# Kernel tuning notes

Hardware: AMD Instinct MI355X
Metric: run time of the kernel (lower is better)

## Reference

```python
import jax, jax.numpy as jnp
import numpy as np

D_MODEL = 1024
NUM_HEADS = 16
DEPTH = D_MODEL // NUM_HEADS
B, S = 2, 2048


def setup_inputs() -> dict:
    key = jax.random.key(0)
    ks = jax.random.split(key, 13)
    sc = 1.0 / np.sqrt(D_MODEL)
    inp = {
        "q": jax.random.normal(ks[0], (B, S, D_MODEL), jnp.float32),
        "k": jax.random.normal(ks[1], (B, S, D_MODEL), jnp.float32),
        "v": jax.random.normal(ks[2], (B, S, D_MODEL), jnp.float32),
        "mask": jax.random.randint(ks[3], (B, 1, S, S), 0, 2).astype(jnp.float32),
        "wq": jax.random.normal(ks[4], (D_MODEL, D_MODEL), jnp.float32) * sc,
        "bq": jnp.zeros((D_MODEL,), jnp.float32),
        "wk": jax.random.normal(ks[5], (D_MODEL, D_MODEL), jnp.float32) * sc,
        "bk": jnp.zeros((D_MODEL,), jnp.float32),
        "wv": jax.random.normal(ks[6], (D_MODEL, D_MODEL), jnp.float32) * sc,
        "bv": jnp.zeros((D_MODEL,), jnp.float32),
        "wo": jax.random.normal(ks[7], (D_MODEL, D_MODEL), jnp.float32) * sc,
        "bo": jnp.zeros((D_MODEL,), jnp.float32),
    }
    return inp


def _split_heads(x):
    # [B,S,D] -> [B,H,S,depth]
    b, s, _ = x.shape
    return x.reshape(b, s, NUM_HEADS, DEPTH).transpose(0, 2, 1, 3)


def reference(q, k, v, mask, wq, bq, wk, bk, wv, bv, wo, bo):
    qh = _split_heads(q @ wq.T + bq)
    kh = _split_heads(k @ wk.T + bk)
    vh = _split_heads(v @ wv.T + bv)
    logits = jnp.einsum("bhqd,bhkd->bhqk", qh, kh) / jnp.sqrt(
        jnp.asarray(DEPTH, jnp.float32))
    logits = logits + mask * (-1e9)
    attn = jax.nn.softmax(logits, axis=-1)
    out = jnp.einsum("bhqk,bhkd->bhqd", attn, vh)
    out = out.transpose(0, 2, 1, 3).reshape(q.shape[0], -1, D_MODEL)
    return out @ wo.T + bo
```

## Files before the change

kernel.cpp:

```cpp
#include <hip/hip_runtime.h>

#define D_MODEL 1024
#define NHEADS  16
#define DEPTH   64
#define BATCH   2
#define SEQ     2048
#define MROWS   (BATCH * SEQ)
#define QSCALE  0.18033688011112042f

typedef unsigned short u16;
typedef unsigned int   u32;
typedef unsigned long long u64;
typedef __bf16 bf16x8 __attribute__((ext_vector_type(8)));
typedef float  f32x4  __attribute__((ext_vector_type(4)));

#if __has_builtin(__builtin_amdgcn_exp2f)
#define EXP2(x) __builtin_amdgcn_exp2f(x)
#else
#define EXP2(x) exp2f(x)
#endif

__device__ __forceinline__ u16 f2b(float f) {
    return __builtin_bit_cast(u16, static_cast<__bf16>(f));
}
__device__ __forceinline__ bf16x8 ldb8(const u16* p) {
    return __builtin_bit_cast(bf16x8, *(const uint4*)p);
}
__device__ __forceinline__ void gload16(const u16* g, u16* l) {
    __builtin_amdgcn_global_load_lds(
        (const __attribute__((address_space(1))) void*)g,
        (__attribute__((address_space(3))) void*)l, 16, 0, 0);
}

__global__ __launch_bounds__(256) void pack_mask(
    const float* __restrict__ mask, u64* __restrict__ bits)
{
    const int w    = blockIdx.x * 4 + (threadIdx.x >> 6);
    const int lane = threadIdx.x & 63;
    float m = mask[(size_t)w * 64 + lane];
    u64 b = __ballot(m > 0.5f);
    if (lane == 0) bits[w] = b;
}

__global__ __launch_bounds__(256) void cvt_bf16(
    const float* __restrict__ q, const float* __restrict__ k, const float* __restrict__ v,
    const float* __restrict__ wq, const float* __restrict__ wk, const float* __restrict__ wv,
    const float* __restrict__ wo,
    u16* __restrict__ xb, u16* __restrict__ wb)
{
    const size_t e = ((size_t)blockIdx.x * 256 + threadIdx.x) * 8;
    const float* src;
    u16* dst;
    size_t off;
    if (e < 12582912) {
        const int a = (int)(e >> 22);
        off = e & 4194303;
        src = (a == 0) ? q : (a == 1) ? k : v;
        dst = xb + ((size_t)a << 22) + off;
    } else {
        const size_t e2 = e - 12582912;
        const int a = (int)(e2 >> 20);
        off = e2 & 1048575;
        src = (a == 0) ? wq : (a == 1) ? wk : (a == 2) ? wv : wo;
        dst = wb + ((size_t)a << 20) + off;
    }
    const float4 f0 = *(const float4*)(src + off);
    const float4 f1 = *(const float4*)(src + off + 4);
    uint4 o;
    o.x = (u32)f2b(f0.x) | ((u32)f2b(f0.y) << 16);
    o.y = (u32)f2b(f0.z) | ((u32)f2b(f0.w) << 16);
    o.z = (u32)f2b(f1.x) | ((u32)f2b(f1.y) << 16);
    o.w = (u32)f2b(f1.z) | ((u32)f2b(f1.w) << 16);
    *(uint4*)dst = o;
}

__global__ __launch_bounds__(256, 3) void proj3_bf16(
    const u16* __restrict__ xb, const u16* __restrict__ wb,
    const float* __restrict__ bq, const float* __restrict__ bk, const float* __restrict__ bv,
    u16* __restrict__ qws, u16* __restrict__ kws, u16* __restrict__ vtws)
{
    __shared__ __align__(16) u16 la[2][128 * 32];
    __shared__ __align__(16) u16 lb[2][128 * 32];

    const int z = blockIdx.z;
    const u16* X = xb + ((size_t)z << 22);
    const u16* W = wb + ((size_t)z << 20);
    const float* Bi = (z == 0) ? bq : (z == 1) ? bk : bv;
    u16* dst       = (z == 0) ? qws : (z == 1) ? kws : vtws;

    const int tid  = threadIdx.x;
    const int wv_  = tid >> 6;
    const int lane = tid & 63;
    const int quad = lane >> 4;
    const int l15  = lane & 15;
    const int bx = blockIdx.y >> 2;
    const int by = (blockIdx.x << 2) | (blockIdx.y & 3);
    const int wm = (wv_ >> 1) * 64;
    const int wn = (wv_ & 1) * 64;

    f32x4 acc[4][4];
    for (int i = 0; i < 4; ++i)
        for (int j = 0; j < 4; ++j)
            acc[i][j] = (f32x4){0.f, 0.f, 0.f, 0.f};

    const int rowA0 = by * 128;
    const int rowB0 = bx * 128;

    const int strow = tid >> 2;
    const int stcol = (tid & 3) * 8;
    const u16* gA0 = &X[(size_t)(rowA0 + strow) * D_MODEL + stcol];
    const u16* gA1 = gA0 + (size_t)64 * D_MODEL;
    const u16* gB0 = &W[(size_t)(rowB0 + strow) * D_MODEL + stcol];
    const u16* gB1 = gB0 + (size_t)64 * D_MODEL;
    const int l0 = tid * 8, l1 = 2048 + tid * 8;

    gload16(gA0, &la[0][l0]);
    gload16(gA1, &la[0][l1]);
    gload16(gB0, &lb[0][l0]);
    gload16(gB1, &lb[0][l1]);
    __syncthreads();

    for (int t = 0; t < 32; ++t) {
        const int buf = t & 1;
        if (t < 31) {
            const int ko = (t + 1) * 32;
            gload16(gA0 + ko, &la[buf ^ 1][l0]);
            gload16(gA1 + ko, &la[buf ^ 1][l1]);
            gload16(gB0 + ko, &lb[buf ^ 1][l0]);
            gload16(gB1 + ko, &lb[buf ^ 1][l1]);
        }
        bf16x8 af[4], bfr[4];
        #pragma unroll
        for (int tt = 0; tt < 4; ++tt) {
            af[tt]  = ldb8(&la[buf][(wm + tt * 16 + l15) * 32 + quad * 8]);
            bfr[tt] = ldb8(&lb[buf][(wn + tt * 16 + l15) * 32 + quad * 8]);
        }
        #pragma unroll
        for (int mt = 0; mt < 4; ++mt)
            #pragma unroll
            for (int nt = 0; nt < 4; ++nt)
                acc[mt][nt] = __builtin_amdgcn_mfma_f32_16x16x32_bf16(af[mt], bfr[nt], acc[mt][nt], 0, 0, 0);
        __syncthreads();
    }

    #pragma unroll
    for (int nt = 0; nt < 4; ++nt) {
        int n = bx * 128 + wn + nt * 16 + l15;
        float bvv = Bi[n];
        int h = n >> 6, d = n & 63;
        #pragma unroll
        for (int mt = 0; mt < 4; ++mt) {
            #pragma unroll
            for (int r = 0; r < 4; ++r) {
                int m = by * 128 + wm + mt * 16 + quad * 4 + r;
                float c = acc[mt][nt][r] + bvv;
                if (z == 0) c *= QSCALE;
                int b = m >> 11, s = m & (SEQ - 1);
                if (z != 2)
                    dst[(((size_t)(b * NHEADS + h) * SEQ) + s) * DEPTH + d] = f2b(c);
                else
                    dst[(((size_t)(b * NHEADS + h) * DEPTH) + d) * SEQ + s] = f2b(c);
            }
        }
    }
}

__global__ __launch_bounds__(256, 3) void proj3_fused(
    const float* __restrict__ q, const float* __restrict__ k, const float* __restrict__ v,
    const float* __restrict__ wq, const float* __restrict__ wk, const float* __restrict__ wv,
    const float* __restrict__ bq, const float* __restrict__ bk, const float* __restrict__ bv,
    u16* __restrict__ qws, u16* __restrict__ kws, u16* __restrict__ vtws)
{
    __shared__ __align__(16) u16 ldsA[128 * 40];
    __shared__ __align__(16) u16 ldsB[128 * 40];

    const int z = blockIdx.z;
    const float* X  = (z == 0) ? q  : (z == 1) ? k  : v;
    const float* W  = (z == 0) ? wq : (z == 1) ? wk : wv;
    const float* Bi = (z == 0) ? bq : (z == 1) ? bk : bv;
    u16* dst        = (z == 0) ? qws : (z == 1) ? kws : vtws;

    const int tid  = threadIdx.x;
    const int wv_  = tid >> 6;
    const int lane = tid & 63;
    const int quad = lane >> 4;
    const int l15  = lane & 15;
    const int bx = blockIdx.y >> 2;
    const int by = (blockIdx.x << 2) | (blockIdx.y & 3);
    const int wm = (wv_ >> 1) * 64;
    const int wn = (wv_ & 1) * 64;

    f32x4 acc[4][4];
    for (int i = 0; i < 4; ++i)
        for (int j = 0; j < 4; ++j)
            acc[i][j] = (f32x4){0.f, 0.f, 0.f, 0.f};

    const int rowA0 = by * 128;
    const int rowB0 = bx * 128;

    const int sr = tid >> 3;
    const int sc = (tid & 7) * 4;

    float4 pa[4], pb[4];
    #pragma unroll
    for (int i = 0; i < 4; ++i) {
        pa[i] = *(const float4*)&X[(size_t)(rowA0 + sr + i * 32) * D_MODEL + sc];
        pb[i] = *(const float4*)&W[(size_t)(rowB0 + sr + i * 32) * D_MODEL + sc];
    }

    for (int it = 0; it < 32; ++it) {
        #pragma unroll
        for (int i = 0; i < 4; ++i) {
            ushort4 ha, hb;
            ha.x = f2b(pa[i].x); ha.y = f2b(pa[i].y); ha.z = f2b(pa[i].z); ha.w = f2b(pa[i].w);
            hb.x = f2b(pb[i].x); hb.y = f2b(pb[i].y); hb.z = f2b(pb[i].z); hb.w = f2b(pb[i].w);
            *(ushort4*)&ldsA[(sr + i * 32) * 40 + sc] = ha;
            *(ushort4*)&ldsB[(sr + i * 32) * 40 + sc] = hb;
        }
        __syncthreads();

        if (it < 31) {
            const int k0 = (it + 1) * 32;
            #pragma unroll
            for (int i = 0; i < 4; ++i) {
                pa[i] = *(const float4*)&X[(size_t)(rowA0 + sr + i * 32) * D_MODEL + k0 + sc];
                pb[i] = *(const float4*)&W[(size_t)(rowB0 + sr + i * 32) * D_MODEL + k0 + sc];
            }
        }

        bf16x8 af[4], bfr[4];
        #pragma unroll
        for (int t = 0; t < 4; ++t) {
            af[t]  = ldb8(&ldsA[(wm + t * 16 + l15) * 40 + quad * 8]);
            bfr[t] = ldb8(&ldsB[(wn + t * 16 + l15) * 40 + quad * 8]);
        }
        #pragma unroll
        for (int mt = 0; mt < 4; ++mt)
            #pragma unroll
            for (int nt = 0; nt < 4; ++nt)
                acc[mt][nt] = __builtin_amdgcn_mfma_f32_16x16x32_bf16(af[mt], bfr[nt], acc[mt][nt], 0, 0, 0);
        __syncthreads();
    }

    #pragma unroll
    for (int nt = 0; nt < 4; ++nt) {
        int n = bx * 128 + wn + nt * 16 + l15;
        float bvv = Bi[n];
        int h = n >> 6, d = n & 63;
        #pragma unroll
        for (int mt = 0; mt < 4; ++mt) {
            #pragma unroll
            for (int r = 0; r < 4; ++r) {
                int m = by * 128 + wm + mt * 16 + quad * 4 + r;
                float c = acc[mt][nt][r] + bvv;
                if (z == 0) c *= QSCALE;
                int b = m >> 11, s = m & (SEQ - 1);
                if (z != 2)
                    dst[(((size_t)(b * NHEADS + h) * SEQ) + s) * DEPTH + d] = f2b(c);
                else
                    dst[(((size_t)(b * NHEADS + h) * DEPTH) + d) * SEQ + s] = f2b(c);
            }
        }
    }
}

__global__ __launch_bounds__(256, 2) void gemm_out_bf16(
    const u16* __restrict__ X, const u16* __restrict__ W,
    const float* __restrict__ bias, float* __restrict__ out)
{
    __shared__ __align__(16) u16 la[2][128 * 32];
    __shared__ __align__(16) u16 lb[2][64 * 32];

    const int tid  = threadIdx.x;
    const int wv_  = tid >> 6;
    const int lane = tid & 63;
    const int quad = lane >> 4;
    const int l15  = lane & 15;
    const int bx = ((blockIdx.y >> 2) << 1) | (blockIdx.x >> 3);
    const int by = ((blockIdx.x & 7) << 2) | (blockIdx.y & 3);
    const int wm = (wv_ >> 1) * 64;
    const int wn = (wv_ & 1) * 32;

    f32x4 acc[4][2];
    for (int i = 0; i < 4; ++i)
        for (int j = 0; j < 2; ++j)
            acc[i][j] = (f32x4){0.f, 0.f, 0.f, 0.f};

    const int rowA0 = by * 128;
    const int rowB0 = bx * 64;

    const int strow = tid >> 2;
    const int stcol = (tid & 3) * 8;
    const u16* gA0 = &X[(size_t)(rowA0 + strow) * D_MODEL + stcol];
    const u16* gA1 = gA0 + (size_t)64 * D_MODEL;
    const u16* gB0 = &W[(size_t)(rowB0 + strow) * D_MODEL + stcol];
    const int l0 = tid * 8, l1 = 2048 + tid * 8;

    gload16(gA0, &la[0][l0]);
    gload16(gA1, &la[0][l1]);
    gload16(gB0, &lb[0][l0]);
    __syncthreads();

    for (int t = 0; t < 32; ++t) {
        const int buf = t & 1;
        if (t < 31) {
            const int ko = (t + 1) * 32;
            gload16(gA0 + ko, &la[buf ^ 1][l0]);
            gload16(gA1 + ko, &la[buf ^ 1][l1]);
            gload16(gB0 + ko, &lb[buf ^ 1][l0]);
        }
        bf16x8 af[4], bfr[2];
        #pragma unroll
        for (int tt = 0; tt < 4; ++tt)
            af[tt] = ldb8(&la[buf][(wm + tt * 16 + l15) * 32 + quad * 8]);
        #pragma unroll
        for (int tt = 0; tt < 2; ++tt)
            bfr[tt] = ldb8(&lb[buf][(wn + tt * 16 + l15) * 32 + quad * 8]);
        #pragma unroll
        for (int mt = 0; mt < 4; ++mt)
            #pragma unroll
            for (int nt = 0; nt < 2; ++nt)
                acc[mt][nt] = __builtin_amdgcn_mfma_f32_16x16x32_bf16(af[mt], bfr[nt], acc[mt][nt], 0, 0, 0);
        __syncthreads();
    }

    #pragma unroll
    for (int nt = 0; nt < 2; ++nt) {
        int n = bx * 64 + wn + nt * 16 + l15;
        float bvv = bias[n];
        #pragma unroll
        for (int mt = 0; mt < 4; ++mt) {
            #pragma unroll
            for (int r = 0; r < 4; ++r) {
                int m = by * 128 + wm + mt * 16 + quad * 4 + r;
                out[(size_t)m * D_MODEL + n] = acc[mt][nt][r] + bvv;
            }
        }
    }
}

__global__ __launch_bounds__(256) void gemm_out_f32(
    const u16* __restrict__ X, const float* __restrict__ W,
    const float* __restrict__ bias, float* __restrict__ out)
{
    __shared__ __align__(16) u16 ldsA[128 * 40];
    __shared__ __align__(16) u16 ldsB[64 * 40];

    const int tid  = threadIdx.x;
    const int wv_  = tid >> 6;
    const int lane = tid & 63;
    const int quad = lane >> 4;
    const int l15  = lane & 15;
    const int bx = ((blockIdx.y >> 2) << 1) | (blockIdx.x >> 3);
    const int by = ((blockIdx.x & 7) << 2) | (blockIdx.y & 3);
    const int wm = (wv_ >> 1) * 64;
    const int wn = (wv_ & 1) * 32;

    f32x4 acc[4][2];
    for (int i = 0; i < 4; ++i)
        for (int j = 0; j < 2; ++j)
            acc[i][j] = (f32x4){0.f, 0.f, 0.f, 0.f};

    const int rowA0 = by * 128;
    const int rowB0 = bx * 64;

    const int ar = tid >> 2, akc = (tid & 3) * 8;
    const int br = tid >> 3, bc = (tid & 7) * 4;

    uint4  paA[2];
    float4 paB[2];
    #pragma unroll
    for (int i = 0; i < 2; ++i) {
        paA[i] = *(const uint4*)&X[(size_t)(rowA0 + ar + i * 64) * D_MODEL + akc];
        paB[i] = *(const float4*)&W[(size_t)(rowB0 + br + i * 32) * D_MODEL + bc];
    }

    for (int it = 0; it < 32; ++it) {
        #pragma unroll
        for (int i = 0; i < 2; ++i) {
            *(uint4*)&ldsA[(ar + i * 64) * 40 + akc] = paA[i];
            ushort4 hb;
            hb.x = f2b(paB[i].x); hb.y = f2b(paB[i].y); hb.z = f2b(paB[i].z); hb.w = f2b(paB[i].w);
            *(ushort4*)&ldsB[(br + i * 32) * 40 + bc] = hb;
        }
        __syncthreads();

        if (it < 31) {
            const int k0 = (it + 1) * 32;
            #pragma unroll
            for (int i = 0; i < 2; ++i) {
                paA[i] = *(const uint4*)&X[(size_t)(rowA0 + ar + i * 64) * D_MODEL + k0 + akc];
                paB[i] = *(const float4*)&W[(size_t)(rowB0 + br + i * 32) * D_MODEL + k0 + bc];
            }
        }

        bf16x8 af[4], bfr[2];
        #pragma unroll
        for (int t = 0; t < 4; ++t)
            af[t] = ldb8(&ldsA[(wm + t * 16 + l15) * 40 + quad * 8]);
        #pragma unroll
        for (int t = 0; t < 2; ++t)
            bfr[t] = ldb8(&ldsB[(wn + t * 16 + l15) * 40 + quad * 8]);
        #pragma unroll
        for (int mt = 0; mt < 4; ++mt)
            #pragma unroll
            for (int nt = 0; nt < 2; ++nt)
                acc[mt][nt] = __builtin_amdgcn_mfma_f32_16x16x32_bf16(af[mt], bfr[nt], acc[mt][nt], 0, 0, 0);
        __syncthreads();
    }

    #pragma unroll
    for (int nt = 0; nt < 2; ++nt) {
        int n = bx * 64 + wn + nt * 16 + l15;
        float bvv = bias[n];
        #pragma unroll
        for (int mt = 0; mt < 4; ++mt) {
            #pragma unroll
            for (int r = 0; r < 4; ++r) {
                int m = by * 128 + wm + mt * 16 + quad * 4 + r;
                out[(size_t)m * D_MODEL + n] = acc[mt][nt][r] + bvv;
            }
        }
    }
}

__global__ __launch_bounds__(256, 2) void flash_attn(
    const u16* __restrict__ Q, const u16* __restrict__ K,
    const u16* __restrict__ Vt, const u64* __restrict__ maskbits,
    u16* __restrict__ O)
{
    __shared__ __align__(16) u16 ldsK[2][64 * 64];
    __shared__ __align__(16) u16 ldsV[2][64 * 64];
    __shared__ __align__(16) u16 ldsP[4][32 * 64];

    const int tid  = threadIdx.x;
    const int wv_  = tid >> 6;
    const int lane = tid & 63;
    const int quad = lane >> 4;
    const int l15  = lane & 15;
    const int bh = ((blockIdx.x & 7) << 2) | (blockIdx.y & 3);
    const int qt = ((blockIdx.y >> 2) << 2) | (blockIdx.x >> 3);
    const int b  = bh >> 4, h = bh & 15;
    const int q0 = qt * 128 + wv_ * 32;

    const u16* Qb = Q  + (size_t)bh * SEQ * DEPTH;
    const u16* Kb = K  + (size_t)bh * SEQ * DEPTH;
    const u16* Vb = Vt + (size_t)bh * DEPTH * SEQ;
    const u64* MB = maskbits + (size_t)b * SEQ * (SEQ / 64);

    const int srow = tid >> 3;
    const int sc8  = tid & 7;
    const int swz  = ((sc8 ^ (srow & 7)) * 8);
    const int kdst0 = srow * 64 + swz;
    const int kdst1 = (srow + 32) * 64 + swz;

    const int xk0 = ((quad ^ (l15 & 7)) * 8);
    const int xk1 = (((4 + quad) ^ (l15 & 7)) * 8);

    bf16x8 aq0[2], aq1[2];
    #pragma unroll
    for (int f = 0; f < 2; ++f) {
        aq0[f] = ldb8(&Qb[(q0 + f * 16 + l15) * DEPTH + quad * 8]);
        aq1[f] = ldb8(&Qb[(q0 + f * 16 + l15) * DEPTH + 32 + quad * 8]);
    }

    bf16x8 vones;
    #pragma unroll
    for (int i = 0; i < 8; ++i) vones[i] = (__bf16)1.0f;

    f32x4 oa[2][4];
    #pragma unroll
    for (int f = 0; f < 2; ++f)
        for (int i = 0; i < 4; ++i) oa[f][i] = (f32x4){0.f, 0.f, 0.f, 0.f};
    f32x4 lacc[2];
    lacc[0] = (f32x4){0.f, 0.f, 0.f, 0.f};
    lacc[1] = (f32x4){0.f, 0.f, 0.f, 0.f};

    u16* myP = ldsP[wv_];

    int wpa[4][4];
    #pragma unroll
    for (int cc = 0; cc < 4; ++cc)
        #pragma unroll
        for (int r = 0; r < 4; ++r) {
            const int row  = quad * 4 + r;
            const int colg = cc * 2 + (l15 >> 3);
            wpa[cc][r] = row * 64 + ((colg ^ (row & 7)) * 8) + (l15 & 7);
        }
    int rp0_[2], rp1_[2];
    #pragma unroll
    for (int f = 0; f < 2; ++f) {
        rp0_[f] = (f * 16 + l15) * 64 + ((quad ^ (l15 & 7)) * 8);
        rp1_[f] = (f * 16 + l15) * 64 + (((4 + quad) ^ (l15 & 7)) * 8);
    }

    uint4 kreg0 = *(const uint4*)&Kb[(size_t)srow * DEPTH + sc8 * 8];
    uint4 kreg1 = *(const uint4*)&Kb[(size_t)(srow + 32) * DEPTH + sc8 * 8];
    uint4 vreg0 = *(const uint4*)&Vb[(size_t)srow * SEQ + sc8 * 8];
    uint4 vreg1 = *(const uint4*)&Vb[(size_t)(srow + 32) * SEQ + sc8 * 8];

    for (int it = 0; it < 32; ++it) {
        const int buf = it & 1;
        u16* Kl = ldsK[buf];
        u16* Vl = ldsV[buf];

        *(uint4*)&Kl[kdst0] = kreg0;
        *(uint4*)&Kl[kdst1] = kreg1;
        *(uint4*)&Vl[kdst0] = vreg0;
        *(uint4*)&Vl[kdst1] = vreg1;
        __syncthreads();

        if (it < 31) {
            const int kb2 = (it + 1) * 64;
            kreg0 = *(const uint4*)&Kb[(size_t)(kb2 + srow) * DEPTH + sc8 * 8];
            kreg1 = *(const uint4*)&Kb[(size_t)(kb2 + srow + 32) * DEPTH + sc8 * 8];
            vreg0 = *(const uint4*)&Vb[(size_t)srow * SEQ + kb2 + sc8 * 8];
            vreg1 = *(const uint4*)&Vb[(size_t)(srow + 32) * SEQ + kb2 + sc8 * 8];
        }

        u32 tlo[2][4], thi[2][4];
        #pragma unroll
        for (int f = 0; f < 2; ++f)
            #pragma unroll
            for (int r = 0; r < 4; ++r) {
                u64 t = MB[(size_t)(q0 + f * 16 + quad * 4 + r) * (SEQ / 64) + it] >> l15;
                tlo[f][r] = (u32)t;
                thi[f][r] = (u32)(t >> 32);
            }

        #pragma unroll
        for (int cc = 0; cc < 4; ++cc) {
            const int row = cc * 16 + l15;
            bf16x8 bk0 = ldb8(&Kl[row * 64 + xk0]);
            bf16x8 bk1 = ldb8(&Kl[row * 64 + xk1]);
            #pragma unroll
            for (int f = 0; f < 2; ++f) {
                f32x4 z = (f32x4){0.f, 0.f, 0.f, 0.f};
                z = __builtin_amdgcn_mfma_f32_16x16x32_bf16(aq0[f], bk0, z, 0, 0, 0);
                z = __builtin_amdgcn_mfma_f32_16x16x32_bf16(aq1[f], bk1, z, 0, 0, 0);
                #pragma unroll
                for (int r = 0; r < 4; ++r) {
                    u32 w   = (cc < 2) ? tlo[f][r] : thi[f][r];
                    u32 bit = (cc & 1) ? ((w >> 16) & 1u) : (w & 1u);
                    float e = EXP2(z[r]);
                    float p = bit ? 0.f : e;
                    myP[wpa[cc][r] + f * 1024] = f2b(p);
                }
            }
        }

        __builtin_amdgcn_wave_barrier();
        __builtin_amdgcn_s_waitcnt(0xc07f);
        __builtin_amdgcn_wave_barrier();
        bf16x8 pa0[2], pa1[2];
        #pragma unroll
        for (int f = 0; f < 2; ++f) {
            pa0[f] = ldb8(&myP[rp0_[f]]);
            pa1[f] = ldb8(&myP[rp1_[f]]);
        }

        #pragma unroll
        for (int f = 0; f < 2; ++f) {
            lacc[f] = __builtin_amdgcn_mfma_f32_16x16x32_bf16(pa0[f], vones, lacc[f], 0, 0, 0);
            lacc[f] = __builtin_amdgcn_mfma_f32_16x16x32_bf16(pa1[f], vones, lacc[f], 0, 0, 0);
        }

        #pragma unroll
        for (int n = 0; n < 4; ++n) {
            const int row = n * 16 + l15;
            bf16x8 bv0 = ldb8(&Vl[row * 64 + xk0]);
            bf16x8 bv1 = ldb8(&Vl[row * 64 + xk1]);
            #pragma unroll
            for (int f = 0; f < 2; ++f) {
                oa[f][n] = __builtin_amdgcn_mfma_f32_16x16x32_bf16(pa0[f], bv0, oa[f][n], 0, 0, 0);
                oa[f][n] = __builtin_amdgcn_mfma_f32_16x16x32_bf16(pa1[f], bv1, oa[f][n], 0, 0, 0);
            }
        }
    }

    #pragma unroll
    for (int f = 0; f < 2; ++f) {
        float inv[4];
        #pragma unroll
        for (int r = 0; r < 4; ++r)
            inv[r] = 1.0f / lacc[f][r];
        #pragma unroll
        for (int n = 0; n < 4; ++n)
            #pragma unroll
            for (int r = 0; r < 4; ++r) {
                int m = q0 + f * 16 + quad * 4 + r;
                O[((size_t)b * SEQ + m) * D_MODEL + h * DEPTH + n * 16 + l15] =
                    f2b(oa[f][n][r] * inv[r]);
            }
    }
}

extern "C" void kernel_launch(void* const* d_in, const int* in_sizes, int n_in,
                              void* d_out, int out_size, void* d_ws, size_t ws_size,
                              hipStream_t stream) {
    const float* q    = (const float*)d_in[0];
    const float* k    = (const float*)d_in[1];
    const float* v    = (const float*)d_in[2];
    const float* mask = (const float*)d_in[3];
    const float* wq   = (const float*)d_in[4];
    const float* bq   = (const float*)d_in[5];
    const float* wk   = (const float*)d_in[6];
    const float* bk   = (const float*)d_in[7];
    const float* wv   = (const float*)d_in[8];
    const float* bv   = (const float*)d_in[9];
    const float* wo   = (const float*)d_in[10];
    const float* bo   = (const float*)d_in[11];

    u16* base = (u16*)d_ws;
    const size_t seg = (size_t)BATCH * NHEADS * SEQ * DEPTH;
    u16* qws  = base;
    u16* kws  = base + seg;
    u16* vtws = base + 2 * seg;
    u16* ows  = base + 3 * seg;
    u64* mbits = (u64*)(base + 4 * seg);
    u16* xb   = base + 4 * seg + 524288;
    u16* wb   = xb + 3 * seg;
    const size_t need_bytes = (4 * seg + 524288 + 3 * seg + 4u * 1048576) * 2;
    const bool bf16path = (ws_size >= need_bytes);

    dim3 blk(256);
    hipLaunchKernelGGL(pack_mask, dim3(BATCH * SEQ * (SEQ / 64) / 4), blk, 0, stream, mask, mbits);

    dim3 gp(D_MODEL / 128, MROWS / 128, 3);
    if (bf16path) {
        hipLaunchKernelGGL(cvt_bf16, dim3(8192), blk, 0, stream,
                           q, k, v, wq, wk, wv, wo, xb, wb);
        hipLaunchKernelGGL(proj3_bf16, gp, blk, 0, stream,
                           xb, wb, bq, bk, bv, qws, kws, vtws);
    } else {
        hipLaunchKernelGGL(proj3_fused, gp, blk, 0, stream,
                           q, k, v, wq, wk, wv, bq, bk, bv, qws, kws, vtws);
    }

    dim3 ga(32, 16);
    hipLaunchKernelGGL(flash_attn, ga, blk, 0, stream, qws, kws, vtws, mbits, ows);

    dim3 go(D_MODEL / 64, MROWS / 128);
    if (bf16path) {
        hipLaunchKernelGGL(gemm_out_bf16, go, blk, 0, stream, ows, wb + 3 * 1048576, bo, (float*)d_out);
    } else {
        hipLaunchKernelGGL(gemm_out_f32, go, blk, 0, stream, ows, wo, bo, (float*)d_out);
    }
}
```

Measured before the change: 285.5 us.

## Split attention across two KV halves and combine partial outputs

Adds a split-KV flash attention kernel that processes each query tile against half of the key sequence, doubling the grid. It writes fp32 partial outputs and row sums, which a new combine kernel adds, normalizes and converts to bf16. The softmax has no running max; it relies on exp2 of the scaled logits staying in range, and row sums come from an MFMA against a ones vector. The intent is more parallelism and occupancy, at the cost of extra global traffic for the fp32 partials, an extra launch, and reuse of the xb workspace region after the projections.

```diff
diff --git a/kernel.cpp b/kernel.cpp
--- a/kernel.cpp
+++ b/kernel.cpp
@@ -424,6 +424,208 @@
     }
 }
 
+__global__ __launch_bounds__(256, 4) void flash_attn_split(
+    const u16* __restrict__ Q, const u16* __restrict__ K,
+    const u16* __restrict__ Vt, const u64* __restrict__ maskbits,
+    float* __restrict__ Opart, float* __restrict__ lpart)
+{
+    __shared__ __align__(16) u16 ldsK[64 * 64];
+    __shared__ __align__(16) u16 ldsV[64 * 64];
+    __shared__ __align__(16) u16 ldsP[4][32 * 64];
+
+    const int tid  = threadIdx.x;
+    const int wv_  = tid >> 6;
+    const int lane = tid & 63;
+    const int quad = lane >> 4;
+    const int l15  = lane & 15;
+    const int bh  = ((blockIdx.x & 7) << 2) | (blockIdx.y & 3);
+    const int qt5 = ((blockIdx.y >> 2) << 2) | (blockIdx.x >> 3);
+    const int qt  = qt5 >> 1;
+    const int kvh = qt5 & 1;
+    const int b  = bh >> 4;
+    const int q0 = qt * 128 + wv_ * 32;
+    const int c0 = kvh * (SEQ / 2);
+
+    const u16* Qb = Q  + (size_t)bh * SEQ * DEPTH;
+    const u16* Kb = K  + (size_t)bh * SEQ * DEPTH;
+    const u16* Vb = Vt + (size_t)bh * DEPTH * SEQ;
+    const u64* MB = maskbits + (size_t)b * SEQ * (SEQ / 64);
+
+    const int srow = tid >> 3;
+    const int sc8  = tid & 7;
+    const int swz  = ((sc8 ^ (srow & 7)) * 8);
+    const int kdst0 = srow * 64 + swz;
+    const int kdst1 = (srow + 32) * 64 + swz;
+
+    const int xk0 = ((quad ^ (l15 & 7)) * 8);
+    const int xk1 = (((4 + quad) ^ (l15 & 7)) * 8);
+
+    bf16x8 aq0[2], aq1[2];
+    #pragma unroll
+    for (int f = 0; f < 2; ++f) {
+        aq0[f] = ldb8(&Qb[(q0 + f * 16 + l15) * DEPTH + quad * 8]);
+        aq1[f] = ldb8(&Qb[(q0 + f * 16 + l15) * DEPTH + 32 + quad * 8]);
+    }
+
+    bf16x8 vones;
+    #pragma unroll
+    for (int i = 0; i < 8; ++i) vones[i] = (__bf16)1.0f;
+
+    f32x4 oa[2][4];
+    #pragma unroll
+    for (int f = 0; f < 2; ++f)
+        for (int i = 0; i < 4; ++i) oa[f][i] = (f32x4){0.f, 0.f, 0.f, 0.f};
+    f32x4 lacc[2];
+    lacc[0] = (f32x4){0.f, 0.f, 0.f, 0.f};
+    lacc[1] = (f32x4){0.f, 0.f, 0.f, 0.f};
+
+    u16* myP = ldsP[wv_];
+
+    int wpa[4][4];
+    #pragma unroll
+    for (int cc = 0; cc < 4; ++cc)
+        #pragma unroll
+        for (int r = 0; r < 4; ++r) {
+            const int row  = quad * 4 + r;
+            const int colg = cc * 2 + (l15 >> 3);
+            wpa[cc][r] = row * 64 + ((colg ^ (row & 7)) * 8) + (l15 & 7);
+        }
+    int rp0_[2], rp1_[2];
+    #pragma unroll
+    for (int f = 0; f < 2; ++f) {
+        rp0_[f] = (f * 16 + l15) * 64 + ((quad ^ (l15 & 7)) * 8);
+        rp1_[f] = (f * 16 + l15) * 64 + (((4 + quad) ^ (l15 & 7)) * 8);
+    }
+
+    uint4 kreg0 = *(const uint4*)&Kb[(size_t)(c0 + srow) * DEPTH + sc8 * 8];
+    uint4 kreg1 = *(const uint4*)&Kb[(size_t)(c0 + srow + 32) * DEPTH + sc8 * 8];
+    uint4 vreg0 = *(const uint4*)&Vb[(size_t)srow * SEQ + c0 + sc8 * 8];
+    uint4 vreg1 = *(const uint4*)&Vb[(size_t)(srow + 32) * SEQ + c0 + sc8 * 8];
+
+    for (int it = 0; it < 16; ++it) {
+        __syncthreads();
+        *(uint4*)&ldsK[kdst0] = kreg0;
+        *(uint4*)&ldsK[kdst1] = kreg1;
+        *(uint4*)&ldsV[kdst0] = vreg0;
+        *(uint4*)&ldsV[kdst1] = vreg1;
+        __syncthreads();
+
+        if (it < 15) {
+            const int cn = c0 + (it + 1) * 64;
+            kreg0 = *(const uint4*)&Kb[(size_t)(cn + srow) * DEPTH + sc8 * 8];
+            kreg1 = *(const uint4*)&Kb[(size_t)(cn + srow + 32) * DEPTH + sc8 * 8];
+            vreg0 = *(const uint4*)&Vb[(size_t)srow * SEQ + cn + sc8 * 8];
+            vreg1 = *(const uint4*)&Vb[(size_t)(srow + 32) * SEQ + cn + sc8 * 8];
+        }
+
+        const int itg = kvh * 16 + it;
+        u32 tlo[2][4], thi[2][4];
+        #pragma unroll
+        for (int f = 0; f < 2; ++f)
+            #pragma unroll
+            for (int r = 0; r < 4; ++r) {
+                u64 t = MB[(size_t)(q0 + f * 16 + quad * 4 + r) * (SEQ / 64) + itg] >> l15;
+                tlo[f][r] = (u32)t;
+                thi[f][r] = (u32)(t >> 32);
+            }
+
+        #pragma unroll
+        for (int cc = 0; cc < 4; ++cc) {
+            const int row = cc * 16 + l15;
+            bf16x8 bk0 = ldb8(&ldsK[row * 64 + xk0]);
+            bf16x8 bk1 = ldb8(&ldsK[row * 64 + xk1]);
+            #pragma unroll
+            for (int f = 0; f < 2; ++f) {
+                f32x4 z = (f32x4){0.f, 0.f, 0.f, 0.f};
+                z = __builtin_amdgcn_mfma_f32_16x16x32_bf16(aq0[f], bk0, z, 0, 0, 0);
+                z = __builtin_amdgcn_mfma_f32_16x16x32_bf16(aq1[f], bk1, z, 0, 0, 0);
+                #pragma unroll
+                for (int r = 0; r < 4; ++r) {
+                    u32 w   = (cc < 2) ? tlo[f][r] : thi[f][r];
+                    u32 bit = (cc & 1) ? ((w >> 16) & 1u) : (w & 1u);
+                    float e = EXP2(z[r]);
+                    float p = bit ? 0.f : e;
+                    myP[wpa[cc][r] + f * 1024] = f2b(p);
+                }
+            }
+        }
+
+        __builtin_amdgcn_wave_barrier();
+        __builtin_amdgcn_s_waitcnt(0xc07f);
+        __builtin_amdgcn_wave_barrier();
+        bf16x8 pa0[2], pa1[2];
+        #pragma unroll
+        for (int f = 0; f < 2; ++f) {
+            pa0[f] = ldb8(&myP[rp0_[f]]);
+            pa1[f] = ldb8(&myP[rp1_[f]]);
+        }
+
+        #pragma unroll
+        for (int f = 0; f < 2; ++f) {
+            lacc[f] = __builtin_amdgcn_mfma_f32_16x16x32_bf16(pa0[f], vones, lacc[f], 0, 0, 0);
+            lacc[f] = __builtin_amdgcn_mfma_f32_16x16x32_bf16(pa1[f], vones, lacc[f], 0, 0, 0);
+        }
+
+        #pragma unroll
+        for (int n = 0; n < 4; ++n) {
+            const int row = n * 16 + l15;
+            bf16x8 bv0 = ldb8(&ldsV[row * 64 + xk0]);
+            bf16x8 bv1 = ldb8(&ldsV[row * 64 + xk1]);
+            #pragma unroll
+            for (int f = 0; f < 2; ++f) {
+                oa[f][n] = __builtin_amdgcn_mfma_f32_16x16x32_bf16(pa0[f], bv0, oa[f][n], 0, 0, 0);
+                oa[f][n] = __builtin_amdgcn_mfma_f32_16x16x32_bf16(pa1[f], bv1, oa[f][n], 0, 0, 0);
+            }
+        }
+    }
+
+    if (l15 == 0) {
+        #pragma unroll
+        for (int f = 0; f < 2; ++f)
+            #pragma unroll
+            for (int r = 0; r < 4; ++r)
+                lpart[(size_t)kvh * 65536 + (size_t)bh * SEQ + q0 + f * 16 + quad * 4 + r] = lacc[f][r];
+    }
+    #pragma unroll
+    for (int f = 0; f < 2; ++f)
+        #pragma unroll
+        for (int n = 0; n < 4; ++n)
+            #pragma unroll
+            for (int r = 0; r < 4; ++r) {
+                const int m = q0 + f * 16 + quad * 4 + r;
+                Opart[(((size_t)kvh * 32 + bh) * SEQ + m) * DEPTH + n * 16 + l15] = oa[f][n][r];
+            }
+}
+
+__global__ __launch_bounds__(256) void combine_o(
+    const float* __restrict__ Op, const float* __restrict__ lp,
+    u16* __restrict__ ows)
+{
+    const size_t idx = ((size_t)blockIdx.x * 256 + threadIdx.x) * 8;
+    const int row = (int)(idx >> 6);
+    const int d0  = (int)(idx & 63);
+    const float* p0 = Op + (size_t)row * 64 + d0;
+    const float4 a0 = *(const float4*)p0;
+    const float4 a1 = *(const float4*)(p0 + 4);
+    const float4 b0 = *(const float4*)(p0 + 4194304);
+    const float4 b1 = *(const float4*)(p0 + 4194308);
+    const float inv = 1.0f / (lp[row] + lp[65536 + row]);
+    const int bh = row >> 11, s = row & 2047;
+    const int b = bh >> 4, h = bh & 15;
+    u16* o = ows + ((size_t)b * SEQ + s) * D_MODEL + h * DEPTH + d0;
+    ushort4 w0, w1;
+    w0.x = f2b((a0.x + b0.x) * inv);
+    w0.y = f2b((a0.y + b0.y) * inv);
+    w0.z = f2b((a0.z + b0.z) * inv);
+    w0.w = f2b((a0.w + b0.w) * inv);
+    w1.x = f2b((a1.x + b1.x) * inv);
+    w1.y = f2b((a1.y + b1.y) * inv);
+    w1.z = f2b((a1.z + b1.z) * inv);
+    w1.w = f2b((a1.w + b1.w) * inv);
+    *(ushort4*)o = w0;
+    *(ushort4*)(o + 4) = w1;
+}
+
 __global__ __launch_bounds__(256, 2) void flash_attn(
     const u16* __restrict__ Q, const u16* __restrict__ K,
     const u16* __restrict__ Vt, const u64* __restrict__ maskbits,
@@ -618,10 +820,15 @@
     u16* vtws = base + 2 * seg;
     u16* ows  = base + 3 * seg;
     u64* mbits = (u64*)(base + 4 * seg);
-    u16* xb   = base + 4 * seg + 524288;
-    u16* wb   = xb + 3 * seg;
-    const size_t need_bytes = (4 * seg + 524288 + 3 * seg + 4u * 1048576) * 2;
-    const bool bf16path = (ws_size >= need_bytes);
+    u16* wb   = base + 4 * seg + 524288;
+    u16* xb   = wb + 4 * 1048576;
+    float* Opart = (float*)xb;
+    float* lpart = Opart + 8388608;
+    const size_t off_xb_u16 = 4 * seg + 524288 + 4 * 1048576;
+    const size_t need_bf16  = (off_xb_u16 + 3 * seg) * 2;
+    const size_t need_split = off_xb_u16 * 2 + (8388608u + 131072u) * 4;
+    const bool bf16path  = (ws_size >= need_bf16);
+    const bool splitpath = bf16path && (ws_size >= need_split);
 
     dim3 blk(256);
     hipLaunchKernelGGL(pack_mask, dim3(BATCH * SEQ * (SEQ / 64) / 4), blk, 0, stream, mask, mbits);
@@ -637,8 +844,15 @@
                            q, k, v, wq, wk, wv, bq, bk, bv, qws, kws, vtws);
     }
 
-    dim3 ga(32, 16);
-    hipLaunchKernelGGL(flash_attn, ga, blk, 0, stream, qws, kws, vtws, mbits, ows);
+    if (splitpath) {
+        dim3 ga(32, 32);
+        hipLaunchKernelGGL(flash_attn_split, ga, blk, 0, stream,
+                           qws, kws, vtws, mbits, Opart, lpart);
+        hipLaunchKernelGGL(combine_o, dim3(2048), blk, 0, stream, Opart, lpart, ows);
+    } else {
+        dim3 ga(32, 16);
+        hipLaunchKernelGGL(flash_attn, ga, blk, 0, stream, qws, kws, vtws, mbits, ows);
+    }
 
     dim3 go(D_MODEL / 64, MROWS / 128);
     if (bf16path) {
```

New measurement: 295.9 us. 1.04x slower.

## Shrink flash-attention query tile, raise occupancy, and coalesce transposed V stores via LDS

Applied to the files above, without the earlier changes.

Flash attention now gives each wave 16 query rows instead of 32, doubling the grid and raising launch bounds to 4 blocks per CU. The intent is more parallelism and occupancy on the attention stage. The cost is that each K/V tile loaded into LDS is reused by half as many queries. Separately, the bf16 projection stages the V output tile through swizzled LDS so the transposed V layout is written with 16-byte coalesced stores instead of scattered 2-byte writes. The workspace order of the bf16 weight and activation buffers is also swapped.

```diff
diff --git a/kernel.cpp b/kernel.cpp
--- a/kernel.cpp
+++ b/kernel.cpp
@@ -79,8 +79,9 @@
     const float* __restrict__ bq, const float* __restrict__ bk, const float* __restrict__ bv,
     u16* __restrict__ qws, u16* __restrict__ kws, u16* __restrict__ vtws)
 {
-    __shared__ __align__(16) u16 la[2][128 * 32];
-    __shared__ __align__(16) u16 lb[2][128 * 32];
+    __shared__ __align__(16) u16 smem[16384];
+    u16 (*la)[4096] = reinterpret_cast<u16(*)[4096]>(smem);
+    u16 (*lb)[4096] = reinterpret_cast<u16(*)[4096]>(smem + 8192);
 
     const int z = blockIdx.z;
     const u16* X = xb + ((size_t)z << 22);
@@ -143,6 +144,134 @@
         __syncthreads();
     }
 
+    if (z != 2) {
+        #pragma unroll
+        for (int nt = 0; nt < 4; ++nt) {
+            int n = rowB0 + wn + nt * 16 + l15;
+            float bvv = Bi[n];
+            int h = n >> 6, d = n & 63;
+            #pragma unroll
+            for (int mt = 0; mt < 4; ++mt) {
+                #pragma unroll
+                for (int r = 0; r < 4; ++r) {
+                    int m = rowA0 + wm + mt * 16 + quad * 4 + r;
+                    float c = acc[mt][nt][r] + bvv;
+                    if (z == 0) c *= QSCALE;
+                    int b = m >> 11, s = m & (SEQ - 1);
+                    dst[(((size_t)(b * NHEADS + h) * SEQ) + s) * DEPTH + d] = f2b(c);
+                }
+            }
+        }
+    } else {
+        #pragma unroll
+        for (int nt = 0; nt < 4; ++nt) {
+            const int nl = wn + nt * 16 + l15;
+            const float bvv = Bi[rowB0 + nl];
+            #pragma unroll
+            for (int mt = 0; mt < 4; ++mt) {
+                #pragma unroll
+                for (int r2 = 0; r2 < 4; r2 += 2) {
+                    const int ml = wm + mt * 16 + quad * 4 + r2;
+                    u32 pk = (u32)f2b(acc[mt][nt][r2] + bvv)
+                           | ((u32)f2b(acc[mt][nt][r2 + 1] + bvv) << 16);
+                    const int g = ml >> 3;
+                    *(u32*)&smem[nl * 128 + (((g ^ (nl & 15)) << 3) | (ml & 7))] = pk;
+                }
+            }
+        }
+        __syncthreads();
+        const int nl  = tid >> 1;
+        const int cc0 = (tid & 1) * 64;
+        const int n   = rowB0 + nl;
+        const int bb  = rowA0 >> 11;
+        u16* dbase = dst + (((size_t)(bb * NHEADS + (n >> 6)) * DEPTH) + (n & 63)) * SEQ
+                   + (rowA0 & (SEQ - 1)) + cc0;
+        #pragma unroll
+        for (int j = 0; j < 8; ++j) {
+            const int g = (tid & 1) * 8 + j;
+            *(uint4*)&dbase[j * 8] =
+                *(const uint4*)&smem[nl * 128 + ((g ^ (nl & 15)) << 3)];
+        }
+    }
+}
+
+__global__ __launch_bounds__(256, 3) void proj3_fused(
+    const float* __restrict__ q, const float* __restrict__ k, const float* __restrict__ v,
+    const float* __restrict__ wq, const float* __restrict__ wk, const float* __restrict__ wv,
+    const float* __restrict__ bq, const float* __restrict__ bk, const float* __restrict__ bv,
+    u16* __restrict__ qws, u16* __restrict__ kws, u16* __restrict__ vtws)
+{
+    __shared__ __align__(16) u16 ldsA[128 * 40];
+    __shared__ __align__(16) u16 ldsB[128 * 40];
+
+    const int z = blockIdx.z;
+    const float* X  = (z == 0) ? q  : (z == 1) ? k  : v;
+    const float* W  = (z == 0) ? wq : (z == 1) ? wk : wv;
+    const float* Bi = (z == 0) ? bq : (z == 1) ? bk : bv;
+    u16* dst        = (z == 0) ? qws : (z == 1) ? kws : vtws;
+
+    const int tid  = threadIdx.x;
+    const int wv_  = tid >> 6;
+    const int lane = tid & 63;
+    const int quad = lane >> 4;
+    const int l15  = lane & 15;
+    const int bx = blockIdx.y >> 2;
+    const int by = (blockIdx.x << 2) | (blockIdx.y & 3);
+    const int wm = (wv_ >> 1) * 64;
+    const int wn = (wv_ & 1) * 64;
+
+    f32x4 acc[4][4];
+    for (int i = 0; i < 4; ++i)
+        for (int j = 0; j < 4; ++j)
+            acc[i][j] = (f32x4){0.f, 0.f, 0.f, 0.f};
+
+    const int rowA0 = by * 128;
+    const int rowB0 = bx * 128;
+
+    const int sr = tid >> 3;
+    const int sc = (tid & 7) * 4;
+
+    float4 pa[4], pb[4];
+    #pragma unroll
+    for (int i = 0; i < 4; ++i) {
+        pa[i] = *(const float4*)&X[(size_t)(rowA0 + sr + i * 32) * D_MODEL + sc];
+        pb[i] = *(const float4*)&W[(size_t)(rowB0 + sr + i * 32) * D_MODEL + sc];
+    }
+
+    for (int it = 0; it < 32; ++it) {
+        #pragma unroll
+        for (int i = 0; i < 4; ++i) {
+            ushort4 ha, hb;
+            ha.x = f2b(pa[i].x); ha.y = f2b(pa[i].y); ha.z = f2b(pa[i].z); ha.w = f2b(pa[i].w);
+            hb.x = f2b(pb[i].x); hb.y = f2b(pb[i].y); hb.z = f2b(pb[i].z); hb.w = f2b(pb[i].w);
+            *(ushort4*)&ldsA[(sr + i * 32) * 40 + sc] = ha;
+            *(ushort4*)&ldsB[(sr + i * 32) * 40 + sc] = hb;
+        }
+        __syncthreads();
+
+        if (it < 31) {
+            const int k0 = (it + 1) * 32;
+            #pragma unroll
+            for (int i = 0; i < 4; ++i) {
+                pa[i] = *(const float4*)&X[(size_t)(rowA0 + sr + i * 32) * D_MODEL + k0 + sc];
+                pb[i] = *(const float4*)&W[(size_t)(rowB0 + sr + i * 32) * D_MODEL + k0 + sc];
+            }
+        }
+
+        bf16x8 af[4], bfr[4];
+        #pragma unroll
+        for (int t = 0; t < 4; ++t) {
+            af[t]  = ldb8(&ldsA[(wm + t * 16 + l15) * 40 + quad * 8]);
+            bfr[t] = ldb8(&ldsB[(wn + t * 16 + l15) * 40 + quad * 8]);
+        }
+        #pragma unroll
+        for (int mt = 0; mt < 4; ++mt)
+            #pragma unroll
+            for (int nt = 0; nt < 4; ++nt)
+                acc[mt][nt] = __builtin_amdgcn_mfma_f32_16x16x32_bf16(af[mt], bfr[nt], acc[mt][nt], 0, 0, 0);
+        __syncthreads();
+    }
+
     #pragma unroll
     for (int nt = 0; nt < 4; ++nt) {
         int n = bx * 128 + wn + nt * 16 + l15;
@@ -165,105 +294,6 @@
     }
 }
 
-__global__ __launch_bounds__(256, 3) void proj3_fused(
-    const float* __restrict__ q, const float* __restrict__ k, const float* __restrict__ v,
-    const float* __restrict__ wq, const float* __restrict__ wk, const float* __restrict__ wv,
-    const float* __restrict__ bq, const float* __restrict__ bk, const float* __restrict__ bv,
-    u16* __restrict__ qws, u16* __restrict__ kws, u16* __restrict__ vtws)
-{
-    __shared__ __align__(16) u16 ldsA[128 * 40];
-    __shared__ __align__(16) u16 ldsB[128 * 40];
-
-    const int z = blockIdx.z;
-    const float* X  = (z == 0) ? q  : (z == 1) ? k  : v;
-    const float* W  = (z == 0) ? wq : (z == 1) ? wk : wv;
-    const float* Bi = (z == 0) ? bq : (z == 1) ? bk : bv;
-    u16* dst        = (z == 0) ? qws : (z == 1) ? kws : vtws;
-
-    const int tid  = threadIdx.x;
-    const int wv_  = tid >> 6;
-    const int lane = tid & 63;
-    const int quad = lane >> 4;
-    const int l15  = lane & 15;
-    const int bx = blockIdx.y >> 2;
-    const int by = (blockIdx.x << 2) | (blockIdx.y & 3);
-    const int wm = (wv_ >> 1) * 64;
-    const int wn = (wv_ & 1) * 64;
-
-    f32x4 acc[4][4];
-    for (int i = 0; i < 4; ++i)
-        for (int j = 0; j < 4; ++j)
-            acc[i][j] = (f32x4){0.f, 0.f, 0.f, 0.f};
-
-    const int rowA0 = by * 128;
-    const int rowB0 = bx * 128;
-
-    const int sr = tid >> 3;
-    const int sc = (tid & 7) * 4;
-
-    float4 pa[4], pb[4];
-    #pragma unroll
-    for (int i = 0; i < 4; ++i) {
-        pa[i] = *(const float4*)&X[(size_t)(rowA0 + sr + i * 32) * D_MODEL + sc];
-        pb[i] = *(const float4*)&W[(size_t)(rowB0 + sr + i * 32) * D_MODEL + sc];
-    }
-
-    for (int it = 0; it < 32; ++it) {
-        #pragma unroll
-        for (int i = 0; i < 4; ++i) {
-            ushort4 ha, hb;
-            ha.x = f2b(pa[i].x); ha.y = f2b(pa[i].y); ha.z = f2b(pa[i].z); ha.w = f2b(pa[i].w);
-            hb.x = f2b(pb[i].x); hb.y = f2b(pb[i].y); hb.z = f2b(pb[i].z); hb.w = f2b(pb[i].w);
-            *(ushort4*)&ldsA[(sr + i * 32) * 40 + sc] = ha;
-            *(ushort4*)&ldsB[(sr + i * 32) * 40 + sc] = hb;
-        }
-        __syncthreads();
-
-        if (it < 31) {
-            const int k0 = (it + 1) * 32;
-            #pragma unroll
-            for (int i = 0; i < 4; ++i) {
-                pa[i] = *(const float4*)&X[(size_t)(rowA0 + sr + i * 32) * D_MODEL + k0 + sc];
-                pb[i] = *(const float4*)&W[(size_t)(rowB0 + sr + i * 32) * D_MODEL + k0 + sc];
-            }
-        }
-
-        bf16x8 af[4], bfr[4];
-        #pragma unroll
-        for (int t = 0; t < 4; ++t) {
-            af[t]  = ldb8(&ldsA[(wm + t * 16 + l15) * 40 + quad * 8]);
-            bfr[t] = ldb8(&ldsB[(wn + t * 16 + l15) * 40 + quad * 8]);
-        }
-        #pragma unroll
-        for (int mt = 0; mt < 4; ++mt)
-            #pragma unroll
-            for (int nt = 0; nt < 4; ++nt)
-                acc[mt][nt] = __builtin_amdgcn_mfma_f32_16x16x32_bf16(af[mt], bfr[nt], acc[mt][nt], 0, 0, 0);
-        __syncthreads();
-    }
-
-    #pragma unroll
-    for (int nt = 0; nt < 4; ++nt) {
-        int n = bx * 128 + wn + nt * 16 + l15;
-        float bvv = Bi[n];
-        int h = n >> 6, d = n & 63;
-        #pragma unroll
-        for (int mt = 0; mt < 4; ++mt) {
-            #pragma unroll
-            for (int r = 0; r < 4; ++r) {
-                int m = by * 128 + wm + mt * 16 + quad * 4 + r;
-                float c = acc[mt][nt][r] + bvv;
-                if (z == 0) c *= QSCALE;
-                int b = m >> 11, s = m & (SEQ - 1);
-                if (z != 2)
-                    dst[(((size_t)(b * NHEADS + h) * SEQ) + s) * DEPTH + d] = f2b(c);
-                else
-                    dst[(((size_t)(b * NHEADS + h) * DEPTH) + d) * SEQ + s] = f2b(c);
-            }
-        }
-    }
-}
-
 __global__ __launch_bounds__(256, 2) void gemm_out_bf16(
     const u16* __restrict__ X, const u16* __restrict__ W,
     const float* __restrict__ bias, float* __restrict__ out)
@@ -424,14 +454,14 @@
     }
 }
 
-__global__ __launch_bounds__(256, 2) void flash_attn(
+__global__ __launch_bounds__(256, 4) void flash_attn(
     const u16* __restrict__ Q, const u16* __restrict__ K,
     const u16* __restrict__ Vt, const u64* __restrict__ maskbits,
     u16* __restrict__ O)
 {
     __shared__ __align__(16) u16 ldsK[2][64 * 64];
     __shared__ __align__(16) u16 ldsV[2][64 * 64];
-    __shared__ __align__(16) u16 ldsP[4][32 * 64];
+    __shared__ __align__(16) u16 ldsP[4][16 * 64];
 
     const int tid  = threadIdx.x;
     const int wv_  = tid >> 6;
@@ -441,7 +471,7 @@
     const int bh = ((blockIdx.x & 7) << 2) | (blockIdx.y & 3);
     const int qt = ((blockIdx.y >> 2) << 2) | (blockIdx.x >> 3);
     const int b  = bh >> 4, h = bh & 15;
-    const int q0 = qt * 128 + wv_ * 32;
+    const int q0 = qt * 64 + wv_ * 16;
 
     const u16* Qb = Q  + (size_t)bh * SEQ * DEPTH;
     const u16* Kb = K  + (size_t)bh * SEQ * DEPTH;
@@ -457,42 +487,30 @@
     const int xk0 = ((quad ^ (l15 & 7)) * 8);
     const int xk1 = (((4 + quad) ^ (l15 & 7)) * 8);
 
-    bf16x8 aq0[2], aq1[2];
-    #pragma unroll
-    for (int f = 0; f < 2; ++f) {
-        aq0[f] = ldb8(&Qb[(q0 + f * 16 + l15) * DEPTH + quad * 8]);
-        aq1[f] = ldb8(&Qb[(q0 + f * 16 + l15) * DEPTH + 32 + quad * 8]);
-    }
+    bf16x8 aq0 = ldb8(&Qb[(q0 + l15) * DEPTH + quad * 8]);
+    bf16x8 aq1 = ldb8(&Qb[(q0 + l15) * DEPTH + 32 + quad * 8]);
 
     bf16x8 vones;
     #pragma unroll
     for (int i = 0; i < 8; ++i) vones[i] = (__bf16)1.0f;
 
-    f32x4 oa[2][4];
-    #pragma unroll
-    for (int f = 0; f < 2; ++f)
-        for (int i = 0; i < 4; ++i) oa[f][i] = (f32x4){0.f, 0.f, 0.f, 0.f};
-    f32x4 lacc[2];
-    lacc[0] = (f32x4){0.f, 0.f, 0.f, 0.f};
-    lacc[1] = (f32x4){0.f, 0.f, 0.f, 0.f};
+    f32x4 oa[4];
+    for (int i = 0; i < 4; ++i) oa[i] = (f32x4){0.f, 0.f, 0.f, 0.f};
+    f32x4 lacc = (f32x4){0.f, 0.f, 0.f, 0.f};
 
     u16* myP = ldsP[wv_];
 
-    int wpa[4][4];
+    int wp[4][4];
     #pragma unroll
     for (int cc = 0; cc < 4; ++cc)
         #pragma unroll
         for (int r = 0; r < 4; ++r) {
             const int row  = quad * 4 + r;
             const int colg = cc * 2 + (l15 >> 3);
-            wpa[cc][r] = row * 64 + ((colg ^ (row & 7)) * 8) + (l15 & 7);
-        }
-    int rp0_[2], rp1_[2];
-    #pragma unroll
-    for (int f = 0; f < 2; ++f) {
-        rp0_[f] = (f * 16 + l15) * 64 + ((quad ^ (l15 & 7)) * 8);
-        rp1_[f] = (f * 16 + l15) * 64 + (((4 + quad) ^ (l15 & 7)) * 8);
-    }
+            wp[cc][r] = row * 64 + ((colg ^ (row & 7)) * 8) + (l15 & 7);
+        }
+    const int rp0 = l15 * 64 + ((quad ^ (l15 & 7)) * 8);
+    const int rp1 = l15 * 64 + (((4 + quad) ^ (l15 & 7)) * 8);
 
     uint4 kreg0 = *(const uint4*)&Kb[(size_t)srow * DEPTH + sc8 * 8];
     uint4 kreg1 = *(const uint4*)&Kb[(size_t)(srow + 32) * DEPTH + sc8 * 8];
@@ -518,81 +536,64 @@
             vreg1 = *(const uint4*)&Vb[(size_t)(srow + 32) * SEQ + kb2 + sc8 * 8];
         }
 
-        u32 tlo[2][4], thi[2][4];
-        #pragma unroll
-        for (int f = 0; f < 2; ++f)
-            #pragma unroll
-            for (int r = 0; r < 4; ++r) {
-                u64 t = MB[(size_t)(q0 + f * 16 + quad * 4 + r) * (SEQ / 64) + it] >> l15;
-                tlo[f][r] = (u32)t;
-                thi[f][r] = (u32)(t >> 32);
-            }
+        u32 tlo[4], thi[4];
+        #pragma unroll
+        for (int r = 0; r < 4; ++r) {
+            u64 t = MB[(size_t)(q0 + quad * 4 + r) * (SEQ / 64) + it] >> l15;
+            tlo[r] = (u32)t;
+            thi[r] = (u32)(t >> 32);
+        }
 
         #pragma unroll
         for (int cc = 0; cc < 4; ++cc) {
             const int row = cc * 16 + l15;
             bf16x8 bk0 = ldb8(&Kl[row * 64 + xk0]);
             bf16x8 bk1 = ldb8(&Kl[row * 64 + xk1]);
-            #pragma unroll
-            for (int f = 0; f < 2; ++f) {
-                f32x4 z = (f32x4){0.f, 0.f, 0.f, 0.f};
-                z = __builtin_amdgcn_mfma_f32_16x16x32_bf16(aq0[f], bk0, z, 0, 0, 0);
-                z = __builtin_amdgcn_mfma_f32_16x16x32_bf16(aq1[f], bk1, z, 0, 0, 0);
-                #pragma unroll
-                for (int r = 0; r < 4; ++r) {
-                    u32 w   = (cc < 2) ? tlo[f][r] : thi[f][r];
-                    u32 bit = (cc & 1) ? ((w >> 16) & 1u) : (w & 1u);
-                    float e = EXP2(z[r]);
-                    float p = bit ? 0.f : e;
-                    myP[wpa[cc][r] + f * 1024] = f2b(p);
-                }
+            f32x4 z = (f32x4){0.f, 0.f, 0.f, 0.f};
+            z = __builtin_amdgcn_mfma_f32_16x16x32_bf16(aq0, bk0, z, 0, 0, 0);
+            z = __builtin_amdgcn_mfma_f32_16x16x32_bf16(aq1, bk1, z, 0, 0, 0);
+            #pragma unroll
+            for (int r = 0; r < 4; ++r) {
+                u32 w   = (cc < 2) ? tlo[r] : thi[r];
+                u32 bit = (cc & 1) ? ((w >> 16) & 1u) : (w & 1u);
+                float e = EXP2(z[r]);
+                float p = bit ? 0.f : e;
+                myP[wp[cc][r]] = f2b(p);
             }
         }
 
         __builtin_amdgcn_wave_barrier();
         __builtin_amdgcn_s_waitcnt(0xc07f);
         __builtin_amdgcn_wave_barrier();
-        bf16x8 pa0[2], pa1[2];
-        #pragma unroll
-        for (int f = 0; f < 2; ++f) {
-            pa0[f] = ldb8(&myP[rp0_[f]]);
-            pa1[f] = ldb8(&myP[rp1_[f]]);
-        }
-
-        #pragma unroll
-        for (int f = 0; f < 2; ++f) {
-            lacc[f] = __builtin_amdgcn_mfma_f32_16x16x32_bf16(pa0[f], vones, lacc[f], 0, 0, 0);
-            lacc[f] = __builtin_amdgcn_mfma_f32_16x16x32_bf16(pa1[f], vones, lacc[f], 0, 0, 0);
-        }
+        bf16x8 pa0 = ldb8(&myP[rp0]);
+        bf16x8 pa1 = ldb8(&myP[rp1]);
+
+        lacc = __builtin_amdgcn_mfma_f32_16x16x32_bf16(pa0, vones, lacc, 0, 0, 0);
+        lacc = __builtin_amdgcn_mfma_f32_16x16x32_bf16(pa1, vones, lacc, 0, 0, 0);
 
         #pragma unroll
         for (int n = 0; n < 4; ++n) {
             const int row = n * 16 + l15;
             bf16x8 bv0 = ldb8(&Vl[row * 64 + xk0]);
             bf16x8 bv1 = ldb8(&Vl[row * 64 + xk1]);
-            #pragma unroll
-            for (int f = 0; f < 2; ++f) {
-                oa[f][n] = __builtin_amdgcn_mfma_f32_16x16x32_bf16(pa0[f], bv0, oa[f][n], 0, 0, 0);
-                oa[f][n] = __builtin_amdgcn_mfma_f32_16x16x32_bf16(pa1[f], bv1, oa[f][n], 0, 0, 0);
-            }
-        }
-    }
-
-    #pragma unroll
-    for (int f = 0; f < 2; ++f) {
-        float inv[4];
-        #pragma unroll
-        for (int r = 0; r < 4; ++r)
-            inv[r] = 1.0f / lacc[f][r];
-        #pragma unroll
-        for (int n = 0; n < 4; ++n)
-            #pragma unroll
-            for (int r = 0; r < 4; ++r) {
-                int m = q0 + f * 16 + quad * 4 + r;
-                O[((size_t)b * SEQ + m) * D_MODEL + h * DEPTH + n * 16 + l15] =
-                    f2b(oa[f][n][r] * inv[r]);
-            }
-    }
+            oa[n] = __builtin_amdgcn_mfma_f32_16x16x32_bf16(pa0, bv0, oa[n], 0, 0, 0);
+            oa[n] = __builtin_amdgcn_mfma_f32_16x16x32_bf16(pa1, bv1, oa[n], 0, 0, 0);
+        }
+    }
+
+    float inv[4];
+    #pragma unroll
+    for (int r = 0; r < 4; ++r)
+        inv[r] = 1.0f / lacc[r];
+
+    #pragma unroll
+    for (int n = 0; n < 4; ++n)
+        #pragma unroll
+        for (int r = 0; r < 4; ++r) {
+            int m = q0 + quad * 4 + r;
+            O[((size_t)b * SEQ + m) * D_MODEL + h * DEPTH + n * 16 + l15] =
+                f2b(oa[n][r] * inv[r]);
+        }
 }
 
 extern "C" void kernel_launch(void* const* d_in, const int* in_sizes, int n_in,
@@ -618,10 +619,10 @@
     u16* vtws = base + 2 * seg;
     u16* ows  = base + 3 * seg;
     u64* mbits = (u64*)(base + 4 * seg);
-    u16* xb   = base + 4 * seg + 524288;
-    u16* wb   = xb + 3 * seg;
-    const size_t need_bytes = (4 * seg + 524288 + 3 * seg + 4u * 1048576) * 2;
-    const bool bf16path = (ws_size >= need_bytes);
+    u16* wb   = base + 4 * seg + 524288;
+    u16* xb   = wb + 4 * 1048576;
+    const size_t need_bf16 = (4 * seg + 524288 + 4 * 1048576 + 3 * seg) * 2;
+    const bool bf16path = (ws_size >= need_bf16);
 
     dim3 blk(256);
     hipLaunchKernelGGL(pack_mask, dim3(BATCH * SEQ * (SEQ / 64) / 4), blk, 0, stream, mask, mbits);
@@ -637,7 +638,7 @@
                            q, k, v, wq, wk, wv, bq, bk, bv, qws, kws, vtws);
     }
 
-    dim3 ga(32, 16);
+    dim3 ga(32, 32);
     hipLaunchKernelGGL(flash_attn, ga, blk, 0, stream, qws, kws, vtws, mbits, ows);
 
     dim3 go(D_MODEL / 64, MROWS / 128);
```

Result: faster. 272.4 us (-4.6%).
